# Performance work log

Hardware: AMD Instinct MI355X
Metric: run time of the kernel (lower is better)

Reference implementation:

```python
import jax, jax.numpy as jnp
import numpy as np

B, C, H, W = 16, 1024, 64, 64  # H*W must equal 64*64=4096 per module math
KDIM = 64

def setup_inputs() -> dict:
    key = jax.random.key(0)
    k1, k2 = jax.random.split(key)
    x = jax.random.normal(k1, (B, C, H, W), dtype=jnp.float32)
    martx = jax.random.normal(k2, (1, H * W, KDIM), dtype=jnp.float32) * 0.02
    aphal = jnp.ones((1,), dtype=jnp.float32)
    gamma = jnp.ones((1,), dtype=jnp.float32)
    return {"x": x, "martx": martx, "aphal": aphal, "gamma": gamma}

def reference(x, martx, aphal, gamma):
    b, c, h, w = x.shape
    n = h * w  # 4096
    q = x.reshape(b, c, n)                      # proj_query: (B, C, N)
    kbank = martx[0]                            # (N, 64), shared across batch
    # energy = bmm(q, martx): (B, C, 64)
    energy = jnp.einsum('bcn,nk->bck', q, kbank)
    # inverted max-subtract trick, then scaled softmax over last dim
    energy_new = jnp.max(energy, axis=-1, keepdims=True) - energy
    attention = jax.nn.softmax(aphal[0] * energy_new, axis=-1)  # (B, C, 64)
    # out = bmm(attention, martx^T): (B, C, N)
    out = jnp.einsum('bck,nk->bcn', attention, kbank)
    out = out.reshape(b, c, h, w)
    return gamma[0] * out + x
```

## Files before the change

### kernel.cpp

```cpp
#include <hip/hip_runtime.h>
#include <hip/hip_bf16.h>


using frag_ab = __attribute__((ext_vector_type(8))) short;
using f32x4   = __attribute__((ext_vector_type(4))) float;

#define MFMA16(a, b, c) __builtin_amdgcn_mfma_f32_16x16x32_bf16((a), (b), (c), 0, 0, 0)

static __device__ __forceinline__ unsigned short f2bf_bits(float f) {
    __hip_bfloat16 h = __float2bfloat16(f);
    return *reinterpret_cast<const unsigned short*>(&h);
}
static __device__ __forceinline__ float bf2f(unsigned short u) {
    return __uint_as_float(((unsigned)u) << 16);
}
static __device__ __forceinline__ frag_ab load_frag(const __hip_bfloat16* p) {
    return *reinterpret_cast<const frag_ab*>(p);
}
static __device__ __forceinline__ frag_ab cvt2(float4 a, float4 b) {
    frag_ab r;
    r[0] = (short)f2bf_bits(a.x); r[1] = (short)f2bf_bits(a.y);
    r[2] = (short)f2bf_bits(a.z); r[3] = (short)f2bf_bits(a.w);
    r[4] = (short)f2bf_bits(b.x); r[5] = (short)f2bf_bits(b.y);
    r[6] = (short)f2bf_bits(b.z); r[7] = (short)f2bf_bits(b.w);
    return r;
}

__global__ __launch_bounds__(256) void prep_frags(
        const float* __restrict__ M,
        __hip_bfloat16* __restrict__ MtF, __hip_bfloat16* __restrict__ MbfF) {
    const int w    = threadIdx.x >> 6;
    const int lane = threadIdx.x & 63;
    const int g    = lane >> 4;
    const int r15  = lane & 15;
    const int f    = blockIdx.x * 4 + w;
    if (f < 512) {
        const int slot = f >> 2, t = f & 3;
        frag_ab fr;
#pragma unroll
        for (int j = 0; j < 8; ++j)
            fr[j] = (short)f2bf_bits(M[(size_t)(32 * slot + 8 * g + j) * 64 + 16 * t + r15]);
        *reinterpret_cast<frag_ab*>(MtF + ((size_t)f * 64 + lane) * 8) = fr;
    } else {
        const int f2 = f - 512;
        const float* src = M + (size_t)(16 * (f2 >> 1) + r15) * 64 + 32 * (f2 & 1) + 8 * g;
        float4 a = *reinterpret_cast<const float4*>(src);
        float4 b = *reinterpret_cast<const float4*>(src + 4);
        *reinterpret_cast<frag_ab*>(MbfF + ((size_t)f2 * 64 + lane) * 8) = cvt2(a, b);
    }
}

__global__ __launch_bounds__(512, 2) void ccam_fused(
        const float* __restrict__ x,
        const __hip_bfloat16* __restrict__ MtF,
        const __hip_bfloat16* __restrict__ MbfF,
        const float* __restrict__ aphal,
        const float* __restrict__ gamma,
        float* __restrict__ out) {
    __shared__ __align__(16) char smem[69760];
    float* Ep = (float*)(smem + 65664);

    const int tid  = threadIdx.x;
    const int w    = tid >> 6;
    const int lane = tid & 63;
    const int g    = lane >> 4;
    const int r15  = lane & 15;
    const int r7   = r15 & 7;
    const int rowbase = blockIdx.x * 8;

    const float alpha = aphal[0];
    const float gam   = gamma[0];

    {
        const float* xr = x + (size_t)(rowbase + w) * 4096;
        char* dst = smem + w * 8208;
#pragma unroll
        for (int rnd = 0; rnd < 2; ++rnd) {
            f32x4 v[8];
#pragma unroll
            for (int i = 0; i < 8; ++i)
                v[i] = __builtin_nontemporal_load(
                    reinterpret_cast<const f32x4*>(xr + rnd * 2048 + i * 256 + 4 * lane));
#pragma unroll
            for (int i = 0; i < 8; ++i) {
                ushort4 u;
                u.x = f2bf_bits(v[i][0]); u.y = f2bf_bits(v[i][1]);
                u.z = f2bf_bits(v[i][2]); u.w = f2bf_bits(v[i][3]);
                *reinterpret_cast<ushort4*>(dst + (rnd * 2048 + i * 256 + 4 * lane) * 2) = u;
            }
        }
    }
    __syncthreads();

    const int t1 = w >> 1;
    const int h1 = w & 1;
    f32x4 acc = {0.f, 0.f, 0.f, 0.f};
    {
        const char* arow = smem + r7 * 8208;
        frag_ab Bc = load_frag(MtF + (((size_t)(64 * h1) * 4 + t1) * 64 + lane) * 8);
#pragma unroll 4
        for (int s = 0; s < 64; ++s) {
            frag_ab Bn = Bc;
            if (s < 63)
                Bn = load_frag(MtF + (((size_t)(64 * h1 + s + 1) * 4 + t1) * 64 + lane) * 8);
            frag_ab A = *reinterpret_cast<const frag_ab*>(
                arow + (h1 * 2048 + 32 * s + 8 * g) * 2);
            acc = MFMA16(A, Bc, acc);
            Bc = Bn;
        }
    }
    if (g < 2) {
#pragma unroll
        for (int reg = 0; reg < 4; ++reg)
            Ep[(((t1 * 2 + h1) * 8) + 4 * g + reg) * 16 + r15] = acc[reg];
    }
    __syncthreads();

    float elo[8], ehi[8];
    {
        const int t0  = g >> 1;
        const int off = 8 * (g & 1);
        const float* e0 = Ep + ((t0 * 2 + 0) * 8 + r7) * 16 + off;
        const float* e1 = Ep + ((t0 * 2 + 1) * 8 + r7) * 16 + off;
        const float* e2 = Ep + (((t0 + 2) * 2 + 0) * 8 + r7) * 16 + off;
        const float* e3 = Ep + (((t0 + 2) * 2 + 1) * 8 + r7) * 16 + off;
        float4 a0 = *reinterpret_cast<const float4*>(e0);
        float4 a1 = *reinterpret_cast<const float4*>(e0 + 4);
        float4 b0 = *reinterpret_cast<const float4*>(e1);
        float4 b1 = *reinterpret_cast<const float4*>(e1 + 4);
        elo[0] = a0.x + b0.x; elo[1] = a0.y + b0.y; elo[2] = a0.z + b0.z; elo[3] = a0.w + b0.w;
        elo[4] = a1.x + b1.x; elo[5] = a1.y + b1.y; elo[6] = a1.z + b1.z; elo[7] = a1.w + b1.w;
        float4 c0 = *reinterpret_cast<const float4*>(e2);
        float4 c1 = *reinterpret_cast<const float4*>(e2 + 4);
        float4 d0 = *reinterpret_cast<const float4*>(e3);
        float4 d1 = *reinterpret_cast<const float4*>(e3 + 4);
        ehi[0] = c0.x + d0.x; ehi[1] = c0.y + d0.y; ehi[2] = c0.z + d0.z; ehi[3] = c0.w + d0.w;
        ehi[4] = c1.x + d1.x; ehi[5] = c1.y + d1.y; ehi[6] = c1.z + d1.z; ehi[7] = c1.w + d1.w;
    }
    float m = elo[0];
#pragma unroll
    for (int j = 1; j < 8; ++j) m = fmaxf(m, elo[j]);
#pragma unroll
    for (int j = 0; j < 8; ++j) m = fmaxf(m, ehi[j]);
    m = fmaxf(m, __shfl_xor(m, 8, 64));
    m = fmaxf(m, __shfl_xor(m, 16, 64));
    m = fmaxf(m, __shfl_xor(m, 32, 64));
#pragma unroll
    for (int j = 0; j < 8; ++j) { elo[j] = alpha * (m - elo[j]); ehi[j] = alpha * (m - ehi[j]); }
    float vm = elo[0];
#pragma unroll
    for (int j = 1; j < 8; ++j) vm = fmaxf(vm, elo[j]);
#pragma unroll
    for (int j = 0; j < 8; ++j) vm = fmaxf(vm, ehi[j]);
    vm = fmaxf(vm, __shfl_xor(vm, 8, 64));
    vm = fmaxf(vm, __shfl_xor(vm, 16, 64));
    vm = fmaxf(vm, __shfl_xor(vm, 32, 64));
    float s = 0.f;
#pragma unroll
    for (int j = 0; j < 8; ++j) { elo[j] = __expf(elo[j] - vm); s += elo[j]; }
#pragma unroll
    for (int j = 0; j < 8; ++j) { ehi[j] = __expf(ehi[j] - vm); s += ehi[j]; }
    s += __shfl_xor(s, 8, 64);
    s += __shfl_xor(s, 16, 64);
    s += __shfl_xor(s, 32, 64);
    const float sc = gam / s;
    frag_ab A0, A1;
#pragma unroll
    for (int j = 0; j < 8; ++j) {
        A0[j] = (short)f2bf_bits(elo[j] * sc);
        A1[j] = (short)f2bf_bits(ehi[j] * sc);
    }

    const int urow0 = 4 * (g & 1);
    const int coff  = (g < 2) ? 0 : 32;
#pragma unroll 1
    for (int gi = 0; gi < 8; ++gi) {
        const int grp = 8 * w + gi;
        frag_ab B[4][2];
#pragma unroll
        for (int t = 0; t < 4; ++t)
#pragma unroll
            for (int h = 0; h < 2; ++h)
                B[t][h] = load_frag(MbfF + (((size_t)(4 * grp + t) * 2 + h) * 64 + lane) * 8);
        f32x4 d0 = {0.f, 0.f, 0.f, 0.f};
        f32x4 d1 = d0, d2 = d0, d3 = d0;
        d0 = MFMA16(A0, B[0][0], d0); d0 = MFMA16(A1, B[0][1], d0);
        d1 = MFMA16(A0, B[1][0], d1); d1 = MFMA16(A1, B[1][1], d1);
        d2 = MFMA16(A0, B[2][0], d2); d2 = MFMA16(A1, B[2][1], d2);
        d3 = MFMA16(A0, B[3][0], d3); d3 = MFMA16(A1, B[3][1], d3);
        f32x4 va, vb;
#pragma unroll
        for (int reg = 0; reg < 4; ++reg) {
            va[reg] = (g < 2) ? d0[reg] : d2[reg];
            vb[reg] = (g < 2) ? d1[reg] : d3[reg];
        }
        const int colbase = grp * 64 + coff + r15;
#pragma unroll
        for (int reg = 0; reg < 4; ++reg) {
            unsigned short* pa =
                (unsigned short*)(smem + (urow0 + reg) * 8208) + colbase;
            unsigned short* pb = pa + 16;
            *pa = f2bf_bits(va[reg] + bf2f(*pa));
            *pb = f2bf_bits(vb[reg] + bf2f(*pb));
        }
    }
    __syncthreads();

    {
        const char* srow = smem + w * 8208;
        float* orow = out + (size_t)(rowbase + w) * 4096;
#pragma unroll
        for (int i = 0; i < 16; ++i) {
            const int col = 256 * i + 4 * lane;
            ushort4 u = *reinterpret_cast<const ushort4*>(srow + col * 2);
            f32x4 v;
            v[0] = bf2f(u.x); v[1] = bf2f(u.y); v[2] = bf2f(u.z); v[3] = bf2f(u.w);
            __builtin_nontemporal_store(v, reinterpret_cast<f32x4*>(orow + col));
        }
    }
}

extern "C" void kernel_launch(void* const* d_in, const int* in_sizes, int n_in,
                              void* d_out, int out_size, void* d_ws, size_t ws_size,
                              hipStream_t stream) {
    const float* x     = (const float*)d_in[0];
    const float* M     = (const float*)d_in[1];
    const float* aphal = (const float*)d_in[2];
    const float* gamma = (const float*)d_in[3];
    __hip_bfloat16* MtF  = (__hip_bfloat16*)d_ws;
    __hip_bfloat16* MbfF = (__hip_bfloat16*)d_ws + 64 * 4096;

    hipLaunchKernelGGL(prep_frags, dim3(256), dim3(256), 0, stream, M, MtF, MbfF);
    hipLaunchKernelGGL(ccam_fused, dim3(2048), dim3(512), 0, stream,
                       x, MtF, MbfF, aphal, gamma, (float*)d_out);
}
```

Baseline: 142.8 us.

## Process 16 rows per block to fill MFMA M dimension and halve B-fragment traffic

```diff
diff --git a/kernel.cpp b/kernel.cpp
--- a/kernel.cpp
+++ b/kernel.cpp
@@ -50,23 +50,22 @@
     }
 }
 
-__global__ __launch_bounds__(512, 2) void ccam_fused(
+__global__ __launch_bounds__(1024, 1) void ccam_fused(
         const float* __restrict__ x,
         const __hip_bfloat16* __restrict__ MtF,
         const __hip_bfloat16* __restrict__ MbfF,
         const float* __restrict__ aphal,
         const float* __restrict__ gamma,
         float* __restrict__ out) {
-    __shared__ __align__(16) char smem[69760];
-    float* Ep = (float*)(smem + 65664);
+    __shared__ __align__(16) char smem[147712];
+    float* Ep = (float*)(smem + 131328);
 
     const int tid  = threadIdx.x;
     const int w    = tid >> 6;
     const int lane = tid & 63;
     const int g    = lane >> 4;
     const int r15  = lane & 15;
-    const int r7   = r15 & 7;
-    const int rowbase = blockIdx.x * 8;
+    const int rowbase = blockIdx.x * 16;
 
     const float alpha = aphal[0];
     const float gam   = gamma[0];
@@ -92,27 +91,29 @@
     }
     __syncthreads();
 
-    const int t1 = w >> 1;
-    const int h1 = w & 1;
-    f32x4 acc = {0.f, 0.f, 0.f, 0.f};
-    {
-        const char* arow = smem + r7 * 8208;
-        frag_ab Bc = load_frag(MtF + (((size_t)(64 * h1) * 4 + t1) * 64 + lane) * 8);
+    const int t1 = w >> 2;
+    const int kq = w & 3;
+    {
+        f32x4 acc = {0.f, 0.f, 0.f, 0.f};
+        const char* arow = smem + r15 * 8208;
+        const int kbase = kq * 1024;
+        const int slot0 = kq * 32;
+        frag_ab Bc = load_frag(MtF + (((size_t)slot0 * 4 + t1) * 64 + lane) * 8);
+        frag_ab Bn = load_frag(MtF + (((size_t)(slot0 + 1) * 4 + t1) * 64 + lane) * 8);
 #pragma unroll 4
-        for (int s = 0; s < 64; ++s) {
-            frag_ab Bn = Bc;
-            if (s < 63)
-                Bn = load_frag(MtF + (((size_t)(64 * h1 + s + 1) * 4 + t1) * 64 + lane) * 8);
+        for (int s = 0; s < 32; ++s) {
+            frag_ab Bn2 = Bn;
+            if (s < 30)
+                Bn2 = load_frag(MtF + (((size_t)(slot0 + s + 2) * 4 + t1) * 64 + lane) * 8);
             frag_ab A = *reinterpret_cast<const frag_ab*>(
-                arow + (h1 * 2048 + 32 * s + 8 * g) * 2);
+                arow + (kbase + 32 * s + 8 * g) * 2);
             acc = MFMA16(A, Bc, acc);
             Bc = Bn;
-        }
-    }
-    if (g < 2) {
+            Bn = Bn2;
+        }
 #pragma unroll
         for (int reg = 0; reg < 4; ++reg)
-            Ep[(((t1 * 2 + h1) * 8) + 4 * g + reg) * 16 + r15] = acc[reg];
+            Ep[(((t1 * 4 + kq) * 16) + 4 * g + reg) * 16 + r15] = acc[reg];
     }
     __syncthreads();
 
@@ -120,29 +121,27 @@
     {
         const int t0  = g >> 1;
         const int off = 8 * (g & 1);
-        const float* e0 = Ep + ((t0 * 2 + 0) * 8 + r7) * 16 + off;
-        const float* e1 = Ep + ((t0 * 2 + 1) * 8 + r7) * 16 + off;
-        const float* e2 = Ep + (((t0 + 2) * 2 + 0) * 8 + r7) * 16 + off;
-        const float* e3 = Ep + (((t0 + 2) * 2 + 1) * 8 + r7) * 16 + off;
-        float4 a0 = *reinterpret_cast<const float4*>(e0);
-        float4 a1 = *reinterpret_cast<const float4*>(e0 + 4);
-        float4 b0 = *reinterpret_cast<const float4*>(e1);
-        float4 b1 = *reinterpret_cast<const float4*>(e1 + 4);
-        elo[0] = a0.x + b0.x; elo[1] = a0.y + b0.y; elo[2] = a0.z + b0.z; elo[3] = a0.w + b0.w;
-        elo[4] = a1.x + b1.x; elo[5] = a1.y + b1.y; elo[6] = a1.z + b1.z; elo[7] = a1.w + b1.w;
-        float4 c0 = *reinterpret_cast<const float4*>(e2);
-        float4 c1 = *reinterpret_cast<const float4*>(e2 + 4);
-        float4 d0 = *reinterpret_cast<const float4*>(e3);
-        float4 d1 = *reinterpret_cast<const float4*>(e3 + 4);
-        ehi[0] = c0.x + d0.x; ehi[1] = c0.y + d0.y; ehi[2] = c0.z + d0.z; ehi[3] = c0.w + d0.w;
-        ehi[4] = c1.x + d1.x; ehi[5] = c1.y + d1.y; ehi[6] = c1.z + d1.z; ehi[7] = c1.w + d1.w;
+#pragma unroll
+        for (int j = 0; j < 8; ++j) { elo[j] = 0.f; ehi[j] = 0.f; }
+#pragma unroll
+        for (int q = 0; q < 4; ++q) {
+            const float* pl = Ep + ((t0 * 4 + q) * 16 + r15) * 16 + off;
+            const float* ph = Ep + (((t0 + 2) * 4 + q) * 16 + r15) * 16 + off;
+            float4 a0 = *reinterpret_cast<const float4*>(pl);
+            float4 a1 = *reinterpret_cast<const float4*>(pl + 4);
+            elo[0] += a0.x; elo[1] += a0.y; elo[2] += a0.z; elo[3] += a0.w;
+            elo[4] += a1.x; elo[5] += a1.y; elo[6] += a1.z; elo[7] += a1.w;
+            float4 c0 = *reinterpret_cast<const float4*>(ph);
+            float4 c1 = *reinterpret_cast<const float4*>(ph + 4);
+            ehi[0] += c0.x; ehi[1] += c0.y; ehi[2] += c0.z; ehi[3] += c0.w;
+            ehi[4] += c1.x; ehi[5] += c1.y; ehi[6] += c1.z; ehi[7] += c1.w;
+        }
     }
     float m = elo[0];
 #pragma unroll
     for (int j = 1; j < 8; ++j) m = fmaxf(m, elo[j]);
 #pragma unroll
     for (int j = 0; j < 8; ++j) m = fmaxf(m, ehi[j]);
-    m = fmaxf(m, __shfl_xor(m, 8, 64));
     m = fmaxf(m, __shfl_xor(m, 16, 64));
     m = fmaxf(m, __shfl_xor(m, 32, 64));
 #pragma unroll
@@ -152,7 +151,6 @@
     for (int j = 1; j < 8; ++j) vm = fmaxf(vm, elo[j]);
 #pragma unroll
     for (int j = 0; j < 8; ++j) vm = fmaxf(vm, ehi[j]);
-    vm = fmaxf(vm, __shfl_xor(vm, 8, 64));
     vm = fmaxf(vm, __shfl_xor(vm, 16, 64));
     vm = fmaxf(vm, __shfl_xor(vm, 32, 64));
     float s = 0.f;
@@ -160,7 +158,6 @@
     for (int j = 0; j < 8; ++j) { elo[j] = __expf(elo[j] - vm); s += elo[j]; }
 #pragma unroll
     for (int j = 0; j < 8; ++j) { ehi[j] = __expf(ehi[j] - vm); s += ehi[j]; }
-    s += __shfl_xor(s, 8, 64);
     s += __shfl_xor(s, 16, 64);
     s += __shfl_xor(s, 32, 64);
     const float sc = gam / s;
@@ -171,11 +168,9 @@
         A1[j] = (short)f2bf_bits(ehi[j] * sc);
     }
 
-    const int urow0 = 4 * (g & 1);
-    const int coff  = (g < 2) ? 0 : 32;
 #pragma unroll 1
-    for (int gi = 0; gi < 8; ++gi) {
-        const int grp = 8 * w + gi;
+    for (int gi = 0; gi < 4; ++gi) {
+        const int grp = 4 * w + gi;
         frag_ab B[4][2];
 #pragma unroll
         for (int t = 0; t < 4; ++t)
@@ -188,20 +183,15 @@
         d1 = MFMA16(A0, B[1][0], d1); d1 = MFMA16(A1, B[1][1], d1);
         d2 = MFMA16(A0, B[2][0], d2); d2 = MFMA16(A1, B[2][1], d2);
         d3 = MFMA16(A0, B[3][0], d3); d3 = MFMA16(A1, B[3][1], d3);
-        f32x4 va, vb;
+        const int colbase = grp * 64 + r15;
 #pragma unroll
         for (int reg = 0; reg < 4; ++reg) {
-            va[reg] = (g < 2) ? d0[reg] : d2[reg];
-            vb[reg] = (g < 2) ? d1[reg] : d3[reg];
-        }
-        const int colbase = grp * 64 + coff + r15;
-#pragma unroll
-        for (int reg = 0; reg < 4; ++reg) {
-            unsigned short* pa =
-                (unsigned short*)(smem + (urow0 + reg) * 8208) + colbase;
-            unsigned short* pb = pa + 16;
-            *pa = f2bf_bits(va[reg] + bf2f(*pa));
-            *pb = f2bf_bits(vb[reg] + bf2f(*pb));
+            unsigned short* p =
+                (unsigned short*)(smem + (4 * g + reg) * 8208) + colbase;
+            p[ 0] = f2bf_bits(d0[reg] + bf2f(p[ 0]));
+            p[16] = f2bf_bits(d1[reg] + bf2f(p[16]));
+            p[32] = f2bf_bits(d2[reg] + bf2f(p[32]));
+            p[48] = f2bf_bits(d3[reg] + bf2f(p[48]));
         }
     }
     __syncthreads();
@@ -231,6 +221,6 @@
     __hip_bfloat16* MbfF = (__hip_bfloat16*)d_ws + 64 * 4096;
 
     hipLaunchKernelGGL(prep_frags, dim3(256), dim3(256), 0, stream, M, MtF, MbfF);
-    hipLaunchKernelGGL(ccam_fused, dim3(2048), dim3(512), 0, stream,
+    hipLaunchKernelGGL(ccam_fused, dim3(1024), dim3(1024), 0, stream,
                        x, MtF, MbfF, aphal, gamma, (float*)d_out);
 }
```

New measurement: 126.5 us, median of 2. -11.4%, faster.
